# Optimization experiments

Hardware: AMD Instinct MI355X
Metric: run time of the kernel (lower is better)

Reference implementation:

```python
import jax, jax.numpy as jnp
import numpy as np

ENT, INNER = 52, 64
BIG = 1e12

def gru_cell(x, h, w_ih, w_hh, b_ih, b_hh):
    # PyTorch GRU gate order: r, z, n
    gi = x @ w_ih.T + b_ih
    gh = h @ w_hh.T + b_hh
    ir, iz, inn = jnp.split(gi, 3, axis=-1)
    hr, hz, hn = jnp.split(gh, 3, axis=-1)
    r = jax.nn.sigmoid(ir + hr)
    z = jax.nn.sigmoid(iz + hz)
    n = jnp.tanh(inn + r * hn)
    return (1.0 - z) * n + z * h

def setup_inputs() -> dict:
    key = jax.random.key(0)
    ks = jax.random.split(key, 16)
    B, S, H = 8, 512, 768
    s = lambda fan: 1.0 / np.sqrt(fan)
    return {
        'last_hidden_state': jax.random.normal(ks[0], (B, S, H), jnp.float32),
        'cls_pooled': jax.random.normal(ks[1], (B, H), jnp.float32),
        'h0': jax.random.normal(ks[2], (2, B, 384), jnp.float32),
        'attention_mask': jnp.ones((B, S), jnp.float32),
        'w_ih_f': jax.random.normal(ks[3], (1152, 768), jnp.float32) * s(768),
        'w_hh_f': jax.random.normal(ks[4], (1152, 384), jnp.float32) * s(384),
        'b_ih_f': jax.random.normal(ks[5], (1152,), jnp.float32) * s(384),
        'b_hh_f': jax.random.normal(ks[6], (1152,), jnp.float32) * s(384),
        'w_ih_b': jax.random.normal(ks[7], (1152, 768), jnp.float32) * s(768),
        'w_hh_b': jax.random.normal(ks[8], (1152, 384), jnp.float32) * s(384),
        'b_ih_b': jax.random.normal(ks[9], (1152,), jnp.float32) * s(384),
        'b_hh_b': jax.random.normal(ks[10], (1152,), jnp.float32) * s(384),
        'dense_w': jax.random.normal(ks[11], (ENT * INNER * 2, 1536), jnp.float32) * s(1536),
        'dense_b': jax.random.normal(ks[12], (ENT * INNER * 2,), jnp.float32) * s(1536),
    }

def reference(last_hidden_state, cls_pooled, h0, attention_mask,
              w_ih_f, w_hh_f, b_ih_f, b_hh_f,
              w_ih_b, w_hh_b, b_ih_b, b_hh_b,
              dense_w, dense_b):
    B, S, H = last_hidden_state.shape
    # bidirectional GRU over a length-1 sequence (the pooled CLS embedding)
    h_fwd = gru_cell(cls_pooled, h0[0], w_ih_f, w_hh_f, b_ih_f, b_hh_f)  # [B,384]
    h_bwd = gru_cell(cls_pooled, h0[1], w_ih_b, w_hh_b, b_ih_b, b_hh_b)  # [B,384]
    cls_emb = jnp.concatenate([h_fwd, h_bwd], axis=-1)                    # [B,768]
    hidden = jnp.concatenate(
        [last_hidden_state, jnp.broadcast_to(cls_emb[:, None, :], (B, S, H))], axis=-1)  # [B,S,1536]
    out = hidden @ dense_w.T + dense_b                                    # [B,S,ENT*2*INNER]
    out = out.reshape(B, S, ENT, 2 * INNER)
    qw, kw = out[..., :INNER], out[..., INNER:]                           # [B,S,ENT,INNER]
    # RoPE (interleaved sin/cos)
    pos = jnp.arange(S, dtype=jnp.float32)[:, None]
    inv_freq = jnp.power(10000.0, -2.0 * jnp.arange(INNER // 2, dtype=jnp.float32) / INNER)
    ang = pos * inv_freq                                                  # [S,INNER/2]
    cos_pos = jnp.repeat(jnp.cos(ang), 2, axis=-1)[None, :, None, :]      # [1,S,1,INNER]
    sin_pos = jnp.repeat(jnp.sin(ang), 2, axis=-1)[None, :, None, :]
    def rot(x):
        x2 = jnp.stack([-x[..., 1::2], x[..., ::2]], axis=-1).reshape(x.shape)
        return x * cos_pos + x2 * sin_pos
    qw, kw = rot(qw), rot(kw)
    logits = jnp.einsum('bmhd,bnhd->bhmn', qw, kw)                        # [B,ENT,S,S]
    pad = attention_mask[:, None, None, :]                                # key-side mask, broadcast
    logits = logits * pad - (1.0 - pad) * BIG
    tril = jnp.tril(jnp.ones((S, S), logits.dtype), -1)
    logits = logits - tril * BIG
    return logits / jnp.sqrt(jnp.float32(INNER))
```

## Files before the change

### kernel.cpp

```cpp
#include <hip/hip_runtime.h>
#include <hip/hip_bf16.h>
#include <math.h>

#define B_    8
#define S_    512
#define H_    768
#define HID_  384
#define G3_   1152
#define ENT_  52
#define INNER_ 64
#define NOUT_ 6656
#define K1_   1536
#define KA_   768
#define BIG_  1000000000000.0f

#define TILE_BYTES 8192
#define A_BLK_BYTES (32u*24u*8192u)
#define B_BLK_BYTES (52u*24u*8192u)
#define QK_BLK_BYTES (8u*52u*4u*2u*8192u)

typedef __attribute__((ext_vector_type(8))) short bf16x8;
typedef __attribute__((ext_vector_type(4))) float f32x4;

__device__ __forceinline__ void splitbf(float x, unsigned& h, unsigned& l) {
    unsigned u = __float_as_uint(x);
    unsigned t = u + 0x7fffu + ((u >> 16) & 1u);
    h = t >> 16;
    float hif = __uint_as_float(t & 0xffff0000u);
    l = __float_as_uint(x - hif) >> 16;
}

__device__ __forceinline__ void gl16(const void* g, void* l) {
    __builtin_amdgcn_global_load_lds((__attribute__((address_space(1))) void*)g,
                                     (__attribute__((address_space(3))) void*)l,
                                     16, 0, 0);
}

__device__ __forceinline__ int tswz(int r, int kk) {
    return (r * 64 + kk * 2) ^ ((r & 7) << 4);
}

__global__ void rope_table_k(float* __restrict__ tab) {
    int idx = blockIdx.x * blockDim.x + threadIdx.x;
    if (idx >= S_ * 32) return;
    int s = idx >> 5;
    int i = idx & 31;
    float invf = powf(10000.0f, -2.0f * (float)i / 64.0f);
    float ang = (float)s * invf;
    tab[idx * 2 + 0] = cosf(ang);
    tab[idx * 2 + 1] = sinf(ang);
}

__global__ void convert_lhs_k(const float* __restrict__ lhs,
                              char* __restrict__ Ah, char* __restrict__ Al) {
    int m = blockIdx.x;
    int t = threadIdx.x;
    float4 v = *reinterpret_cast<const float4*>(&lhs[(size_t)m * KA_ + t * 4]);
    unsigned h0,l0,h1,l1,h2,l2,h3,l3;
    splitbf(v.x, h0, l0); splitbf(v.y, h1, l1);
    splitbf(v.z, h2, l2); splitbf(v.w, h3, l3);
    int bm = m >> 7, r = m & 127;
    int kt = t >> 3, kk = (t & 7) * 4;
    size_t base = ((size_t)bm * 24 + kt) * TILE_BYTES;
    int off = tswz(r, kk);
    uint2 hv = make_uint2(h0 | (h1 << 16), h2 | (h3 << 16));
    uint2 lv = make_uint2(l0 | (l1 << 16), l2 | (l3 << 16));
    *reinterpret_cast<uint2*>(Ah + base + off) = hv;
    *reinterpret_cast<uint2*>(Al + base + off) = lv;
}

__global__ void convert_dw_k(const float* __restrict__ dw,
                             char* __restrict__ Bh, char* __restrict__ Bl) {
    int n = blockIdx.x;
    int t = threadIdx.x;
    float4 v = *reinterpret_cast<const float4*>(&dw[(size_t)n * K1_ + t * 4]);
    unsigned h0,l0,h1,l1,h2,l2,h3,l3;
    splitbf(v.x, h0, l0); splitbf(v.y, h1, l1);
    splitbf(v.z, h2, l2); splitbf(v.w, h3, l3);
    int bn = n >> 7, r = n & 127;
    int kt = t >> 3, kk = (t & 7) * 4;
    size_t base = ((size_t)bn * 24 + kt) * TILE_BYTES;
    int off = tswz(r, kk);
    uint2 hv = make_uint2(h0 | (h1 << 16), h2 | (h3 << 16));
    uint2 lv = make_uint2(l0 | (l1 << 16), l2 | (l3 << 16));
    *reinterpret_cast<uint2*>(Bh + base + off) = hv;
    *reinterpret_cast<uint2*>(Bl + base + off) = lv;
}

__global__ void gru_gemm_k(const float* __restrict__ cls,
                           const float* __restrict__ h0,
                           const float* __restrict__ wihf, const float* __restrict__ whhf,
                           const float* __restrict__ bihf, const float* __restrict__ bhhf,
                           const float* __restrict__ wihb, const float* __restrict__ whhb,
                           const float* __restrict__ bihb, const float* __restrict__ bhhb,
                           float* __restrict__ gi, float* __restrict__ gh) {
    int wave = blockIdx.x * (blockDim.x >> 6) + (threadIdx.x >> 6);
    int lane = threadIdx.x & 63;
    if (wave >= 2 * G3_) return;
    int dir = wave / G3_;
    int j = wave % G3_;
    const float* wih = dir ? wihb : wihf;
    const float* whh = dir ? whhb : whhf;
    const float* bih = dir ? bihb : bihf;
    const float* bhh = dir ? bhhb : bhhf;

    float ai[B_], ah[B_];
#pragma unroll
    for (int b = 0; b < B_; ++b) { ai[b] = 0.f; ah[b] = 0.f; }
    for (int k = lane; k < H_; k += 64) {
        float w = wih[j * H_ + k];
#pragma unroll
        for (int b = 0; b < B_; ++b) ai[b] += w * cls[b * H_ + k];
    }
    for (int k = lane; k < HID_; k += 64) {
        float w = whh[j * HID_ + k];
#pragma unroll
        for (int b = 0; b < B_; ++b) ah[b] += w * h0[(dir * B_ + b) * HID_ + k];
    }
#pragma unroll
    for (int off = 32; off > 0; off >>= 1) {
#pragma unroll
        for (int b = 0; b < B_; ++b) {
            ai[b] += __shfl_xor(ai[b], off);
            ah[b] += __shfl_xor(ah[b], off);
        }
    }
    if (lane == 0) {
#pragma unroll
        for (int b = 0; b < B_; ++b) {
            gi[(dir * B_ + b) * G3_ + j] = ai[b] + bih[j];
            gh[(dir * B_ + b) * G3_ + j] = ah[b] + bhh[j];
        }
    }
}

__global__ void gru_combine_k(const float* __restrict__ gi, const float* __restrict__ gh,
                              const float* __restrict__ h0, float* __restrict__ cls_emb) {
    int idx = blockIdx.x * blockDim.x + threadIdx.x;
    if (idx >= 2 * B_ * HID_) return;
    int dir = idx / (B_ * HID_);
    int r = idx % (B_ * HID_);
    int b = r / HID_;
    int h = r % HID_;
    const float* giP = gi + (dir * B_ + b) * G3_;
    const float* ghP = gh + (dir * B_ + b) * G3_;
    float ir = giP[h],        hr = ghP[h];
    float iz = giP[HID_ + h], hz = ghP[HID_ + h];
    float in_ = giP[2 * HID_ + h], hn = ghP[2 * HID_ + h];
    float rr = 1.f / (1.f + expf(-(ir + hr)));
    float z  = 1.f / (1.f + expf(-(iz + hz)));
    float n  = tanhf(in_ + rr * hn);
    float hp = h0[(dir * B_ + b) * HID_ + h];
    cls_emb[b * H_ + dir * HID_ + h] = (1.f - z) * n + z * hp;
}

__global__ void cls_ctr_k(const float* __restrict__ cls_emb,
                          const float* __restrict__ dw, const float* __restrict__ db,
                          float* __restrict__ ctr) {
    int wave = blockIdx.x * (blockDim.x >> 6) + (threadIdx.x >> 6);
    int lane = threadIdx.x & 63;
    if (wave >= NOUT_) return;
    const float* w = dw + (size_t)wave * K1_ + KA_;
    float a[B_];
#pragma unroll
    for (int b = 0; b < B_; ++b) a[b] = 0.f;
    for (int k = lane; k < H_; k += 64) {
        float ww = w[k];
#pragma unroll
        for (int b = 0; b < B_; ++b) a[b] += ww * cls_emb[b * H_ + k];
    }
#pragma unroll
    for (int off = 32; off > 0; off >>= 1) {
#pragma unroll
        for (int b = 0; b < B_; ++b) a[b] += __shfl_xor(a[b], off);
    }
    if (lane == 0) {
#pragma unroll
        for (int b = 0; b < B_; ++b) ctr[b * NOUT_ + wave] = a[b] + db[wave];
    }
}

__global__ __launch_bounds__(256)
void dense_mfma_k(const char* __restrict__ Ahb, const char* __restrict__ Alb,
                  const char* __restrict__ Bhb, const char* __restrict__ Blb,
                  const float* __restrict__ ctr, const float* __restrict__ rope,
                  char* __restrict__ qh, char* __restrict__ ql,
                  char* __restrict__ kh, char* __restrict__ kl) {
    __shared__ __align__(16) char lds[32768];
    char* ldsAh = lds;
    char* ldsAl = lds + 8192;
    char* ldsBh = lds + 16384;
    char* ldsBl = lds + 24576;

    int tid = threadIdx.x;
    int w = tid >> 6, lane = tid & 63;
    int l15 = lane & 15, l4 = lane >> 4;
    int wr = w >> 1, wc = w & 1;
    int bn = blockIdx.x, bm = blockIdx.y;

    f32x4 acc[4][4] = {};

    const char* Ah0 = Ahb + (size_t)bm * 24 * TILE_BYTES;
    const char* Al0 = Alb + (size_t)bm * 24 * TILE_BYTES;
    const char* Bh0 = Bhb + (size_t)bn * 24 * TILE_BYTES;
    const char* Bl0 = Blb + (size_t)bn * 24 * TILE_BYTES;

    int c0 = w * 1024 + lane * 16;
    int c1 = (w + 4) * 1024 + lane * 16;
    int d0 = w * 1024, d1 = (w + 4) * 1024;

    for (int kt = 0; kt < 24; ++kt) {
        size_t tb = (size_t)kt * TILE_BYTES;
        gl16(Ah0 + tb + c0, ldsAh + d0); gl16(Ah0 + tb + c1, ldsAh + d1);
        gl16(Al0 + tb + c0, ldsAl + d0); gl16(Al0 + tb + c1, ldsAl + d1);
        gl16(Bh0 + tb + c0, ldsBh + d0); gl16(Bh0 + tb + c1, ldsBh + d1);
        gl16(Bl0 + tb + c0, ldsBl + d0); gl16(Bl0 + tb + c1, ldsBl + d1);
        __syncthreads();

        bf16x8 ah[4], al[4], bh[4], bl[4];
#pragma unroll
        for (int mi = 0; mi < 4; ++mi) {
            int row = wr * 64 + mi * 16 + l15;
            int off = (row * 64 + l4 * 16) ^ ((row & 7) << 4);
            ah[mi] = *reinterpret_cast<const bf16x8*>(ldsAh + off);
            al[mi] = *reinterpret_cast<const bf16x8*>(ldsAl + off);
        }
#pragma unroll
        for (int ni = 0; ni < 4; ++ni) {
            int col = wc * 64 + ni * 16 + l15;
            int off = (col * 64 + l4 * 16) ^ ((col & 7) << 4);
            bh[ni] = *reinterpret_cast<const bf16x8*>(ldsBh + off);
            bl[ni] = *reinterpret_cast<const bf16x8*>(ldsBl + off);
        }
#pragma unroll
        for (int mi = 0; mi < 4; ++mi)
#pragma unroll
            for (int ni = 0; ni < 4; ++ni) {
                acc[mi][ni] = __builtin_amdgcn_mfma_f32_16x16x32_bf16(ah[mi], bh[ni], acc[mi][ni], 0, 0, 0);
                acc[mi][ni] = __builtin_amdgcn_mfma_f32_16x16x32_bf16(ah[mi], bl[ni], acc[mi][ni], 0, 0, 0);
                acc[mi][ni] = __builtin_amdgcn_mfma_f32_16x16x32_bf16(al[mi], bh[ni], acc[mi][ni], 0, 0, 0);
            }
        __syncthreads();
    }

    int b = bm >> 2;
    int ent = bn;
    char* DH = wc ? kh : qh;
    char* DL = wc ? kl : ql;
    size_t panel = (size_t)b * ENT_ + ent;
    int tm = bm & 3;
    const float2* rope2 = reinterpret_cast<const float2*>(rope);

#pragma unroll
    for (int ni = 0; ni < 4; ++ni) {
        int d = ni * 16 + l15;
        float ctrv = ctr[b * NOUT_ + ent * 128 + wc * 64 + d];
        int ktq = d >> 5, kk = d & 31;
        size_t base = ((panel * 4 + tm) * 2 + ktq) * TILE_BYTES;
#pragma unroll
        for (int mi = 0; mi < 4; ++mi) {
#pragma unroll
            for (int j = 0; j < 4; ++j) {
                int r = wr * 64 + mi * 16 + l4 * 4 + j;
                int s = tm * 128 + r;
                float v = acc[mi][ni][j] + ctrv;
                float2 cs = rope2[s * 32 + (d >> 1)];
                float p = __shfl_xor(v, 1);
                float o = (d & 1) ? fmaf(p, cs.y, v * cs.x)
                                  : fmaf(-p, cs.y, v * cs.x);
                unsigned hbits, lbits;
                splitbf(o, hbits, lbits);
                int off = tswz(r, kk);
                *reinterpret_cast<unsigned short*>(DH + base + off) = (unsigned short)hbits;
                *reinterpret_cast<unsigned short*>(DL + base + off) = (unsigned short)lbits;
            }
        }
    }
}

__global__ __launch_bounds__(256)
void logits_mfma_k(const char* __restrict__ qh, const char* __restrict__ ql,
                   const char* __restrict__ kh, const char* __restrict__ kl,
                   const float* __restrict__ mask, float* __restrict__ out) {
    __shared__ __align__(16) char lds[32768];
    char* ldsQh = lds;
    char* ldsQl = lds + 8192;
    char* ldsKh = lds + 16384;
    char* ldsKl = lds + 24576;

    int tid = threadIdx.x;
    int w = tid >> 6, lane = tid & 63;
    int l15 = lane & 15, l4 = lane >> 4;
    int wr = w >> 1, wc = w & 1;
    int tile = blockIdx.x;
    int tm = tile >> 2, tn = tile & 3;
    int hh = blockIdx.y, bb = blockIdx.z;
    size_t panel = (size_t)bb * ENT_ + hh;

    f32x4 acc[4][4] = {};

    int c0 = w * 1024 + lane * 16;
    int c1 = (w + 4) * 1024 + lane * 16;
    int d0 = w * 1024, d1 = (w + 4) * 1024;

    for (int kt = 0; kt < 2; ++kt) {
        const char* pQh = qh + ((panel * 4 + tm) * 2 + kt) * TILE_BYTES;
        const char* pQl = ql + ((panel * 4 + tm) * 2 + kt) * TILE_BYTES;
        const char* pKh = kh + ((panel * 4 + tn) * 2 + kt) * TILE_BYTES;
        const char* pKl = kl + ((panel * 4 + tn) * 2 + kt) * TILE_BYTES;
        gl16(pQh + c0, ldsQh + d0); gl16(pQh + c1, ldsQh + d1);
        gl16(pQl + c0, ldsQl + d0); gl16(pQl + c1, ldsQl + d1);
        gl16(pKh + c0, ldsKh + d0); gl16(pKh + c1, ldsKh + d1);
        gl16(pKl + c0, ldsKl + d0); gl16(pKl + c1, ldsKl + d1);
        __syncthreads();

        bf16x8 ah[4], al[4], bh[4], bl[4];
#pragma unroll
        for (int mi = 0; mi < 4; ++mi) {
            int row = wr * 64 + mi * 16 + l15;
            int off = (row * 64 + l4 * 16) ^ ((row & 7) << 4);
            ah[mi] = *reinterpret_cast<const bf16x8*>(ldsQh + off);
            al[mi] = *reinterpret_cast<const bf16x8*>(ldsQl + off);
        }
#pragma unroll
        for (int ni = 0; ni < 4; ++ni) {
            int col = wc * 64 + ni * 16 + l15;
            int off = (col * 64 + l4 * 16) ^ ((col & 7) << 4);
            bh[ni] = *reinterpret_cast<const bf16x8*>(ldsKh + off);
            bl[ni] = *reinterpret_cast<const bf16x8*>(ldsKl + off);
        }
#pragma unroll
        for (int mi = 0; mi < 4; ++mi)
#pragma unroll
            for (int ni = 0; ni < 4; ++ni) {
                acc[mi][ni] = __builtin_amdgcn_mfma_f32_16x16x32_bf16(ah[mi], bh[ni], acc[mi][ni], 0, 0, 0);
                acc[mi][ni] = __builtin_amdgcn_mfma_f32_16x16x32_bf16(ah[mi], bl[ni], acc[mi][ni], 0, 0, 0);
                acc[mi][ni] = __builtin_amdgcn_mfma_f32_16x16x32_bf16(al[mi], bh[ni], acc[mi][ni], 0, 0, 0);
            }
        __syncthreads();
    }

    size_t obase = panel * (size_t)(S_ * S_);
#pragma unroll
    for (int ni = 0; ni < 4; ++ni) {
        int n = tn * 128 + wc * 64 + ni * 16 + l15;
        float p = mask[bb * S_ + n];
        float bigterm = (1.0f - p) * BIG_;
#pragma unroll
        for (int mi = 0; mi < 4; ++mi) {
#pragma unroll
            for (int j = 0; j < 4; ++j) {
                int m = tm * 128 + wr * 64 + mi * 16 + l4 * 4 + j;
                float val = acc[mi][ni][j];
                val = val * p - bigterm;
                if (n < m) val -= BIG_;
                out[obase + (size_t)m * S_ + n] = val * 0.125f;
            }
        }
    }
}

extern "C" void kernel_launch(void* const* d_in, const int* in_sizes, int n_in,
                              void* d_out, int out_size, void* d_ws, size_t ws_size,
                              hipStream_t stream) {
    const float* lhs  = (const float*)d_in[0];
    const float* cls  = (const float*)d_in[1];
    const float* h0   = (const float*)d_in[2];
    const float* mask = (const float*)d_in[3];
    const float* wihf = (const float*)d_in[4];
    const float* whhf = (const float*)d_in[5];
    const float* bihf = (const float*)d_in[6];
    const float* bhhf = (const float*)d_in[7];
    const float* wihb = (const float*)d_in[8];
    const float* whhb = (const float*)d_in[9];
    const float* bihb = (const float*)d_in[10];
    const float* bhhb = (const float*)d_in[11];
    const float* dw   = (const float*)d_in[12];
    const float* db   = (const float*)d_in[13];
    float* out = (float*)d_out;

    char* p = (char*)d_ws;
    char* Ahb = p;  p += A_BLK_BYTES;
    char* Alb = p;  p += A_BLK_BYTES;
    char* Bhb = p;  p += B_BLK_BYTES;
    char* Blb = p;  p += B_BLK_BYTES;
    char* qhb = p;  p += QK_BLK_BYTES;
    char* qlb = p;  p += QK_BLK_BYTES;
    char* khb = p;  p += QK_BLK_BYTES;
    char* klb = p;  p += QK_BLK_BYTES;
    float* gi      = (float*)p;
    float* gh      = gi + 2 * B_ * G3_;
    float* cls_emb = gh + 2 * B_ * G3_;
    float* ctr     = cls_emb + B_ * H_;
    float* rope    = ctr + B_ * NOUT_;

    rope_table_k<<<64, 256, 0, stream>>>(rope);
    convert_lhs_k<<<4096, 192, 0, stream>>>(lhs, Ahb, Alb);
    convert_dw_k<<<6656, 192, 0, stream>>>(dw, Bhb, Blb);
    gru_gemm_k<<<576, 256, 0, stream>>>(cls, h0, wihf, whhf, bihf, bhhf,
                                        wihb, whhb, bihb, bhhb, gi, gh);
    gru_combine_k<<<24, 256, 0, stream>>>(gi, gh, h0, cls_emb);
    cls_ctr_k<<<NOUT_ / 4, 256, 0, stream>>>(cls_emb, dw, db, ctr);
    dense_mfma_k<<<dim3(ENT_, 32), 256, 0, stream>>>(Ahb, Alb, Bhb, Blb,
                                                     ctr, rope, qhb, qlb, khb, klb);
    logits_mfma_k<<<dim3(16, ENT_, B_), 256, 0, stream>>>(qhb, qlb, khb, klb, mask, out);
}
```

Before: 743.1 us.

## Restructure dense and logits MFMA kernels with swapped operands, Q register reuse, vector stores

The dense kernel swaps operand roles so each lane holds four consecutive output dims. That lets its RoPE/split epilogue emit packed 8-byte stores instead of scalar 2-byte stores. The logits kernel keeps the Q fragment in registers and loops over all four K column tiles per block, cutting the grid fourfold. It writes float4 output rows, and both kernels use an XCD-aware block remapping to improve L2 locality. The trade-offs are more registers for the held Q fragments, fewer blocks in the logits launch, and a launch-bounds occupancy hint on the dense kernel.

```diff
diff --git a/kernel.cpp b/kernel.cpp
--- a/kernel.cpp
+++ b/kernel.cpp
@@ -180,7 +180,7 @@
     }
 }
 
-__global__ __launch_bounds__(256)
+__global__ __launch_bounds__(256, 3)
 void dense_mfma_k(const char* __restrict__ Ahb, const char* __restrict__ Alb,
                   const char* __restrict__ Bhb, const char* __restrict__ Blb,
                   const float* __restrict__ ctr, const float* __restrict__ rope,
@@ -196,7 +196,10 @@
     int w = tid >> 6, lane = tid & 63;
     int l15 = lane & 15, l4 = lane >> 4;
     int wr = w >> 1, wc = w & 1;
-    int bn = blockIdx.x, bm = blockIdx.y;
+
+    int flat = blockIdx.x + 52 * blockIdx.y;
+    int nb = (flat & 7) * 208 + (flat >> 3);
+    int bn = nb % 52, bm = nb / 52;
 
     f32x4 acc[4][4] = {};
 
@@ -206,8 +209,8 @@
     const char* Bl0 = Blb + (size_t)bn * 24 * TILE_BYTES;
 
     int c0 = w * 1024 + lane * 16;
-    int c1 = (w + 4) * 1024 + lane * 16;
-    int d0 = w * 1024, d1 = (w + 4) * 1024;
+    int c1 = c0 + 4096;
+    int d0 = w * 1024, d1 = d0 + 4096;
 
     for (int kt = 0; kt < 24; ++kt) {
         size_t tb = (size_t)kt * TILE_BYTES;
@@ -217,63 +220,67 @@
         gl16(Bl0 + tb + c0, ldsBl + d0); gl16(Bl0 + tb + c1, ldsBl + d1);
         __syncthreads();
 
-        bf16x8 ah[4], al[4], bh[4], bl[4];
+        bf16x8 lh[4], ll[4];
+#pragma unroll
+        for (int ni = 0; ni < 4; ++ni) {
+            int row = wr * 64 + ni * 16 + l15;
+            int off = (row * 64 + l4 * 16) ^ ((row & 7) << 4);
+            lh[ni] = *reinterpret_cast<const bf16x8*>(ldsAh + off);
+            ll[ni] = *reinterpret_cast<const bf16x8*>(ldsAl + off);
+        }
 #pragma unroll
         for (int mi = 0; mi < 4; ++mi) {
-            int row = wr * 64 + mi * 16 + l15;
+            int row = wc * 64 + mi * 16 + l15;
             int off = (row * 64 + l4 * 16) ^ ((row & 7) << 4);
-            ah[mi] = *reinterpret_cast<const bf16x8*>(ldsAh + off);
-            al[mi] = *reinterpret_cast<const bf16x8*>(ldsAl + off);
-        }
-#pragma unroll
-        for (int ni = 0; ni < 4; ++ni) {
-            int col = wc * 64 + ni * 16 + l15;
-            int off = (col * 64 + l4 * 16) ^ ((col & 7) << 4);
-            bh[ni] = *reinterpret_cast<const bf16x8*>(ldsBh + off);
-            bl[ni] = *reinterpret_cast<const bf16x8*>(ldsBl + off);
-        }
-#pragma unroll
-        for (int mi = 0; mi < 4; ++mi)
+            bf16x8 wh = *reinterpret_cast<const bf16x8*>(ldsBh + off);
+            bf16x8 wl = *reinterpret_cast<const bf16x8*>(ldsBl + off);
 #pragma unroll
             for (int ni = 0; ni < 4; ++ni) {
-                acc[mi][ni] = __builtin_amdgcn_mfma_f32_16x16x32_bf16(ah[mi], bh[ni], acc[mi][ni], 0, 0, 0);
-                acc[mi][ni] = __builtin_amdgcn_mfma_f32_16x16x32_bf16(ah[mi], bl[ni], acc[mi][ni], 0, 0, 0);
-                acc[mi][ni] = __builtin_amdgcn_mfma_f32_16x16x32_bf16(al[mi], bh[ni], acc[mi][ni], 0, 0, 0);
+                acc[mi][ni] = __builtin_amdgcn_mfma_f32_16x16x32_bf16(wh, lh[ni], acc[mi][ni], 0, 0, 0);
+                acc[mi][ni] = __builtin_amdgcn_mfma_f32_16x16x32_bf16(wh, ll[ni], acc[mi][ni], 0, 0, 0);
+                acc[mi][ni] = __builtin_amdgcn_mfma_f32_16x16x32_bf16(wl, lh[ni], acc[mi][ni], 0, 0, 0);
             }
+        }
         __syncthreads();
     }
 
     int b = bm >> 2;
+    int tm = bm & 3;
     int ent = bn;
     char* DH = wc ? kh : qh;
     char* DL = wc ? kl : ql;
     size_t panel = (size_t)b * ENT_ + ent;
-    int tm = bm & 3;
     const float2* rope2 = reinterpret_cast<const float2*>(rope);
 
 #pragma unroll
-    for (int ni = 0; ni < 4; ++ni) {
-        int d = ni * 16 + l15;
-        float ctrv = ctr[b * NOUT_ + ent * 128 + wc * 64 + d];
-        int ktq = d >> 5, kk = d & 31;
-        size_t base = ((panel * 4 + tm) * 2 + ktq) * TILE_BYTES;
-#pragma unroll
-        for (int mi = 0; mi < 4; ++mi) {
-#pragma unroll
-            for (int j = 0; j < 4; ++j) {
-                int r = wr * 64 + mi * 16 + l4 * 4 + j;
-                int s = tm * 128 + r;
-                float v = acc[mi][ni][j] + ctrv;
-                float2 cs = rope2[s * 32 + (d >> 1)];
-                float p = __shfl_xor(v, 1);
-                float o = (d & 1) ? fmaf(p, cs.y, v * cs.x)
-                                  : fmaf(-p, cs.y, v * cs.x);
-                unsigned hbits, lbits;
-                splitbf(o, hbits, lbits);
-                int off = tswz(r, kk);
-                *reinterpret_cast<unsigned short*>(DH + base + off) = (unsigned short)hbits;
-                *reinterpret_cast<unsigned short*>(DL + base + off) = (unsigned short)lbits;
-            }
+    for (int mi = 0; mi < 4; ++mi) {
+        int dq0 = mi * 16 + l4 * 4;
+        int ktq = dq0 >> 5, kk = dq0 & 31;
+        float4 cv = *reinterpret_cast<const float4*>(
+            &ctr[b * NOUT_ + ent * 128 + wc * 64 + dq0]);
+        size_t tbase = ((panel * 4 + tm) * 2 + ktq) * TILE_BYTES;
+#pragma unroll
+        for (int ni = 0; ni < 4; ++ni) {
+            int r = wr * 64 + ni * 16 + l15;
+            int s = tm * 128 + r;
+            float2 cs01 = rope2[s * 32 + (dq0 >> 1)];
+            float2 cs23 = rope2[s * 32 + (dq0 >> 1) + 1];
+            float v0 = acc[mi][ni][0] + cv.x;
+            float v1 = acc[mi][ni][1] + cv.y;
+            float v2 = acc[mi][ni][2] + cv.z;
+            float v3 = acc[mi][ni][3] + cv.w;
+            float o0 = v0 * cs01.x - v1 * cs01.y;
+            float o1 = v1 * cs01.x + v0 * cs01.y;
+            float o2 = v2 * cs23.x - v3 * cs23.y;
+            float o3 = v3 * cs23.x + v2 * cs23.y;
+            unsigned h0,l0,h1,l1,h2,l2,h3,l3;
+            splitbf(o0, h0, l0); splitbf(o1, h1, l1);
+            splitbf(o2, h2, l2); splitbf(o3, h3, l3);
+            int off = tswz(r, kk);
+            *reinterpret_cast<uint2*>(DH + tbase + off) =
+                make_uint2(h0 | (h1 << 16), h2 | (h3 << 16));
+            *reinterpret_cast<uint2*>(DL + tbase + off) =
+                make_uint2(l0 | (l1 << 16), l2 | (l3 << 16));
         }
     }
 }
@@ -283,80 +290,95 @@
                    const char* __restrict__ kh, const char* __restrict__ kl,
                    const float* __restrict__ mask, float* __restrict__ out) {
     __shared__ __align__(16) char lds[32768];
-    char* ldsQh = lds;
-    char* ldsQl = lds + 8192;
-    char* ldsKh = lds + 16384;
-    char* ldsKl = lds + 24576;
+    char* ldsKh = lds;
+    char* ldsKl = lds + 16384;
 
     int tid = threadIdx.x;
     int w = tid >> 6, lane = tid & 63;
     int l15 = lane & 15, l4 = lane >> 4;
     int wr = w >> 1, wc = w & 1;
-    int tile = blockIdx.x;
-    int tm = tile >> 2, tn = tile & 3;
-    int hh = blockIdx.y, bb = blockIdx.z;
+
+    int flat = blockIdx.x + 4 * (blockIdx.y + 52 * blockIdx.z);
+    int nb = (flat & 7) * 208 + (flat >> 3);
+    int tm = nb & 3;
+    int t2 = nb >> 2;
+    int hh = t2 % 52, bb = t2 / 52;
     size_t panel = (size_t)bb * ENT_ + hh;
 
-    f32x4 acc[4][4] = {};
+    bf16x8 qf_h[2][4], qf_l[2][4];
+    {
+        const char* Qh0 = qh + (panel * 4 + tm) * 2 * TILE_BYTES;
+        const char* Ql0 = ql + (panel * 4 + tm) * 2 * TILE_BYTES;
+#pragma unroll
+        for (int kt = 0; kt < 2; ++kt) {
+#pragma unroll
+            for (int mi = 0; mi < 4; ++mi) {
+                int r = wc * 64 + mi * 16 + l15;
+                int off = kt * TILE_BYTES + tswz(r, l4 * 8);
+                qf_h[kt][mi] = *reinterpret_cast<const bf16x8*>(Qh0 + off);
+                qf_l[kt][mi] = *reinterpret_cast<const bf16x8*>(Ql0 + off);
+            }
+        }
+    }
 
     int c0 = w * 1024 + lane * 16;
-    int c1 = (w + 4) * 1024 + lane * 16;
-    int d0 = w * 1024, d1 = (w + 4) * 1024;
-
-    for (int kt = 0; kt < 2; ++kt) {
-        const char* pQh = qh + ((panel * 4 + tm) * 2 + kt) * TILE_BYTES;
-        const char* pQl = ql + ((panel * 4 + tm) * 2 + kt) * TILE_BYTES;
-        const char* pKh = kh + ((panel * 4 + tn) * 2 + kt) * TILE_BYTES;
-        const char* pKl = kl + ((panel * 4 + tn) * 2 + kt) * TILE_BYTES;
-        gl16(pQh + c0, ldsQh + d0); gl16(pQh + c1, ldsQh + d1);
-        gl16(pQl + c0, ldsQl + d0); gl16(pQl + c1, ldsQl + d1);
-        gl16(pKh + c0, ldsKh + d0); gl16(pKh + c1, ldsKh + d1);
-        gl16(pKl + c0, ldsKl + d0); gl16(pKl + c1, ldsKl + d1);
+    int c1 = c0 + 4096;
+    int d0 = w * 1024, d1 = d0 + 4096;
+    size_t obase = panel * (size_t)(S_ * S_);
+    int m = tm * 128 + wc * 64 + l15;
+
+    for (int tn = 0; tn < 4; ++tn) {
+        const char* Kh0 = kh + (panel * 4 + tn) * 2 * TILE_BYTES;
+        const char* Kl0 = kl + (panel * 4 + tn) * 2 * TILE_BYTES;
+#pragma unroll
+        for (int kt = 0; kt < 2; ++kt) {
+            gl16(Kh0 + kt * TILE_BYTES + c0, ldsKh + kt * TILE_BYTES + d0);
+            gl16(Kh0 + kt * TILE_BYTES + c1, ldsKh + kt * TILE_BYTES + d1);
+            gl16(Kl0 + kt * TILE_BYTES + c0, ldsKl + kt * TILE_BYTES + d0);
+            gl16(Kl0 + kt * TILE_BYTES + c1, ldsKl + kt * TILE_BYTES + d1);
+        }
         __syncthreads();
 
-        bf16x8 ah[4], al[4], bh[4], bl[4];
-#pragma unroll
-        for (int mi = 0; mi < 4; ++mi) {
-            int row = wr * 64 + mi * 16 + l15;
-            int off = (row * 64 + l4 * 16) ^ ((row & 7) << 4);
-            ah[mi] = *reinterpret_cast<const bf16x8*>(ldsQh + off);
-            al[mi] = *reinterpret_cast<const bf16x8*>(ldsQl + off);
-        }
+        f32x4 acc[4][4] = {};
+#pragma unroll
+        for (int kt = 0; kt < 2; ++kt) {
+#pragma unroll
+            for (int ni = 0; ni < 4; ++ni) {
+                int r = wr * 64 + ni * 16 + l15;
+                int off = kt * TILE_BYTES + tswz(r, l4 * 8);
+                bf16x8 ah = *reinterpret_cast<const bf16x8*>(ldsKh + off);
+                bf16x8 al = *reinterpret_cast<const bf16x8*>(ldsKl + off);
+#pragma unroll
+                for (int mi = 0; mi < 4; ++mi) {
+                    acc[mi][ni] = __builtin_amdgcn_mfma_f32_16x16x32_bf16(ah, qf_h[kt][mi], acc[mi][ni], 0, 0, 0);
+                    acc[mi][ni] = __builtin_amdgcn_mfma_f32_16x16x32_bf16(ah, qf_l[kt][mi], acc[mi][ni], 0, 0, 0);
+                    acc[mi][ni] = __builtin_amdgcn_mfma_f32_16x16x32_bf16(al, qf_h[kt][mi], acc[mi][ni], 0, 0, 0);
+                }
+            }
+        }
+
 #pragma unroll
         for (int ni = 0; ni < 4; ++ni) {
-            int col = wc * 64 + ni * 16 + l15;
-            int off = (col * 64 + l4 * 16) ^ ((col & 7) << 4);
-            bh[ni] = *reinterpret_cast<const bf16x8*>(ldsKh + off);
-            bl[ni] = *reinterpret_cast<const bf16x8*>(ldsKl + off);
-        }
-#pragma unroll
-        for (int mi = 0; mi < 4; ++mi)
-#pragma unroll
-            for (int ni = 0; ni < 4; ++ni) {
-                acc[mi][ni] = __builtin_amdgcn_mfma_f32_16x16x32_bf16(ah[mi], bh[ni], acc[mi][ni], 0, 0, 0);
-                acc[mi][ni] = __builtin_amdgcn_mfma_f32_16x16x32_bf16(ah[mi], bl[ni], acc[mi][ni], 0, 0, 0);
-                acc[mi][ni] = __builtin_amdgcn_mfma_f32_16x16x32_bf16(al[mi], bh[ni], acc[mi][ni], 0, 0, 0);
+            int n0 = tn * 128 + wr * 64 + ni * 16 + l4 * 4;
+            float4 p4 = *reinterpret_cast<const float4*>(&mask[bb * S_ + n0]);
+            const float* pv = reinterpret_cast<const float*>(&p4);
+#pragma unroll
+            for (int mi = 0; mi < 4; ++mi) {
+                int mm = m + mi * 16;
+                float4 o;
+                float* ov = reinterpret_cast<float*>(&o);
+#pragma unroll
+                for (int j = 0; j < 4; ++j) {
+                    float val = acc[mi][ni][j];
+                    float p = pv[j];
+                    val = val * p - (1.0f - p) * BIG_;
+                    if (n0 + j < mm) val -= BIG_;
+                    ov[j] = val * 0.125f;
+                }
+                *reinterpret_cast<float4*>(&out[obase + (size_t)mm * S_ + n0]) = o;
             }
+        }
         __syncthreads();
-    }
-
-    size_t obase = panel * (size_t)(S_ * S_);
-#pragma unroll
-    for (int ni = 0; ni < 4; ++ni) {
-        int n = tn * 128 + wc * 64 + ni * 16 + l15;
-        float p = mask[bb * S_ + n];
-        float bigterm = (1.0f - p) * BIG_;
-#pragma unroll
-        for (int mi = 0; mi < 4; ++mi) {
-#pragma unroll
-            for (int j = 0; j < 4; ++j) {
-                int m = tm * 128 + wr * 64 + mi * 16 + l4 * 4 + j;
-                float val = acc[mi][ni][j];
-                val = val * p - bigterm;
-                if (n < m) val -= BIG_;
-                out[obase + (size_t)m * S_ + n] = val * 0.125f;
-            }
-        }
     }
 }
 
@@ -403,5 +425,5 @@
     cls_ctr_k<<<NOUT_ / 4, 256, 0, stream>>>(cls_emb, dw, db, ctr);
     dense_mfma_k<<<dim3(ENT_, 32), 256, 0, stream>>>(Ahb, Alb, Bhb, Blb,
                                                      ctr, rope, qhb, qlb, khb, klb);
-    logits_mfma_k<<<dim3(16, ENT_, B_), 256, 0, stream>>>(qhb, qlb, khb, klb, mask, out);
-}
+    logits_mfma_k<<<dim3(4, ENT_, B_), 256, 0, stream>>>(qhb, qlb, khb, klb, mask, out);
+}
```

Measured after the change: 743.3 us. No clear change (+0.0%).
